# Optimization experiments

Hardware: AMD Instinct MI355X
Metric: run time of the kernel (lower is better)

Reference implementation:

```python
import jax, jax.numpy as jnp
import numpy as np


def setup_inputs() -> dict:
    key = jax.random.key(0)
    k1, k2, k3, k4 = jax.random.split(key, 4)
    B, C, T, H, W = 2, 64, 8, 48, 48
    C2 = C // 2
    x_in = jax.random.normal(k1, (B, C, T, H, W), dtype=jnp.float32)
    # per-time-slice 1x1 conv weights (theta/phi pairs), kaiming-ish scale
    theta_w = jax.random.normal(k2, (T, C2, C), dtype=jnp.float32) / np.sqrt(C)
    phi_w = jax.random.normal(k3, (T, C2, C), dtype=jnp.float32) / np.sqrt(C)
    out_w = jax.random.normal(k4, (C, C), dtype=jnp.float32) / np.sqrt(C)
    return {"x_in": x_in, "theta_w": theta_w, "phi_w": phi_w, "out_w": out_w}


def reference(x_in, theta_w, phi_w, out_w):
    B, C, T, H, W = x_in.shape
    C2 = theta_w.shape[1]
    P = H * W
    # [B, T, C, P] layout: flatten spatial, move time next to batch
    x = jnp.transpose(x_in, (0, 2, 1, 3, 4)).reshape(B, T, C, P)
    # per-slice 1x1 convs == per-slice channel matmuls with slice-specific weights
    theta = jnp.einsum("toc,btcp->btop", theta_w, x)  # [B,T,C2,P]
    phi = jnp.einsum("toc,btcp->btop", phi_w, x)      # [B,T,C2,P]
    scale = 1.0 / jnp.sqrt(jnp.asarray(C2, dtype=x_in.dtype))
    scores = jnp.einsum("btcp,btcq->btpq", theta, phi) * scale  # [B,T,P,P]
    attn = jax.nn.softmax(scores, axis=-1)
    f = jnp.einsum("btpq,btcq->btcp", attn, x)  # value = raw x, [B,T,C,P]
    # conv_out: 1x1x1 Conv3d (pointwise over channels), then residual
    out = jnp.einsum("oc,btcp->btop", out_w, f)
    out = jnp.transpose(out.reshape(B, T, C, H, W), (0, 2, 1, 3, 4))
    return out + x_in
```

## Files before the change

### kernel.cpp

```cpp
#include <hip/hip_runtime.h>
#include <hip/hip_bf16.h>

#define CC 64
#define TT 8
#define PP 2304
#define C2 32
#define BT 16
#define NKT 36
#define SCALE2 0.25503486f

using h8 = __attribute__((ext_vector_type(8))) _Float16;
using h4 = __attribute__((ext_vector_type(4))) _Float16;
using f4 = __attribute__((ext_vector_type(4))) float;

#if __has_builtin(__builtin_amdgcn_exp2f)
#define EXP2(v) __builtin_amdgcn_exp2f(v)
#else
#define EXP2(v) exp2f(v)
#endif

#define SWIZ_BT(xcd, g) ((xcd) + 8 * ((g) & 1))


__global__ __launch_bounds__(512) void k_prep(
    const float* __restrict__ x, const float* __restrict__ tw,
    const float* __restrict__ pw, _Float16* __restrict__ thf,
    _Float16* __restrict__ rec) {
  const int qt = blockIdx.y >> 1, bt = SWIZ_BT(blockIdx.x, blockIdx.y);
  const int b = bt >> 3, t = bt & 7;
  const int tid = threadIdx.x;
  const int wv = tid >> 6, lane = tid & 63;
  const int quad = lane >> 4, l15 = lane & 15;

  __shared__ __align__(16) float x_s[64][68];
  __shared__ __align__(16) _Float16 th_s[4][16][32];
  __shared__ __align__(16) _Float16 ph_s[4][16][32];

  const size_t xslice = ((size_t)b * CC * TT + t) * PP;
  const int qg0 = qt * 64;
  _Float16* rb = rec + (size_t)(bt * NKT + qt) * 6144;
  const f4 zero = {0.f, 0.f, 0.f, 0.f};

  {
    const int l16 = tid & 15;
    const int crow = tid >> 4;
#pragma unroll
    for (int ppass = 0; ppass < 2; ppass++) {
      const int c = ppass * 32 + crow;
      float4 u = *reinterpret_cast<const float4*>(
          &x[xslice + (size_t)c * (TT * PP) + qg0 + l16 * 4]);
      x_s[l16 * 4 + 0][c] = u.x;
      x_s[l16 * 4 + 1][c] = u.y;
      x_s[l16 * 4 + 2][c] = u.z;
      x_s[l16 * 4 + 3][c] = u.w;
    }
  }
  __syncthreads();

  if (wv < 4) {
    h8 bx[2];
#pragma unroll
    for (int ks = 0; ks < 2; ks++) {
      const float* row = &x_s[wv * 16 + l15][ks * 32 + quad * 8];
      float4 u0 = *reinterpret_cast<const float4*>(row);
      float4 u1 = *reinterpret_cast<const float4*>(row + 4);
      bx[ks][0] = (_Float16)u0.x; bx[ks][1] = (_Float16)u0.y;
      bx[ks][2] = (_Float16)u0.z; bx[ks][3] = (_Float16)u0.w;
      bx[ks][4] = (_Float16)u1.x; bx[ks][5] = (_Float16)u1.y;
      bx[ks][6] = (_Float16)u1.z; bx[ks][7] = (_Float16)u1.w;
    }

    const float* twt = tw + t * C2 * CC;
    const float* pwt = pw + t * C2 * CC;
    f4 accT[2] = {zero, zero}, accP[2] = {zero, zero};
#pragma unroll
    for (int mt = 0; mt < 2; mt++)
#pragma unroll
      for (int ks = 0; ks < 2; ks++) {
        const float* wr = twt + (mt * 16 + l15) * CC + ks * 32 + quad * 8;
        const float* pr = pwt + (mt * 16 + l15) * CC + ks * 32 + quad * 8;
        float4 a0 = *reinterpret_cast<const float4*>(wr);
        float4 a1 = *reinterpret_cast<const float4*>(wr + 4);
        float4 p0 = *reinterpret_cast<const float4*>(pr);
        float4 p1 = *reinterpret_cast<const float4*>(pr + 4);
        h8 at = {(_Float16)a0.x, (_Float16)a0.y, (_Float16)a0.z,
                 (_Float16)a0.w, (_Float16)a1.x, (_Float16)a1.y,
                 (_Float16)a1.z, (_Float16)a1.w};
        h8 ap = {(_Float16)p0.x, (_Float16)p0.y, (_Float16)p0.z,
                 (_Float16)p0.w, (_Float16)p1.x, (_Float16)p1.y,
                 (_Float16)p1.z, (_Float16)p1.w};
        accT[mt] = __builtin_amdgcn_mfma_f32_16x16x32_f16(at, bx[ks],
                                                          accT[mt], 0, 0, 0);
        accP[mt] = __builtin_amdgcn_mfma_f32_16x16x32_f16(ap, bx[ks],
                                                          accP[mt], 0, 0, 0);
      }

#pragma unroll
    for (int mt = 0; mt < 2; mt++) {
      h4 tv, pv;
#pragma unroll
      for (int r = 0; r < 4; r++) {
        tv[r] = (_Float16)(accT[mt][r] * SCALE2);
        pv[r] = (_Float16)accP[mt][r];
      }
      *reinterpret_cast<h4*>(&th_s[wv][l15][mt * 16 + quad * 4]) = tv;
      *reinterpret_cast<h4*>(&ph_s[wv][l15][mt * 16 + quad * 4]) = pv;
    }

    h8 tfrag = *reinterpret_cast<const h8*>(&th_s[wv][l15][quad * 8]);
    *reinterpret_cast<h8*>(
        thf + (((size_t)(bt * NKT + qt) * 4 + wv) * 64 + lane) * 8) = tfrag;

    h8 pfrag = *reinterpret_cast<const h8*>(&ph_s[wv][l15][quad * 8]);
    *reinterpret_cast<h8*>(rb + wv * 512 + lane * 8) = pfrag;
  } else {
    const int w2 = wv - 4;
    const int g = w2 >> 1;
#pragma unroll
    for (int ct2 = 0; ct2 < 2; ct2++) {
      const int ct = (w2 & 1) * 2 + ct2;
      h8 v;
#pragma unroll
      for (int j = 0; j < 4; j++) {
        v[j] = (_Float16)x_s[32 * g + quad * 4 + j][ct * 16 + l15];
        v[4 + j] = (_Float16)x_s[32 * g + 16 + quad * 4 + j][ct * 16 + l15];
      }
      *reinterpret_cast<h8*>(rb + 2048 + (g * 4 + ct) * 512 + lane * 8) = v;
    }
  }
}

__global__ __launch_bounds__(192, 3) void k_attn(
    const float* __restrict__ x, const _Float16* __restrict__ thf,
    const _Float16* __restrict__ rec, const float* __restrict__ ow,
    float* __restrict__ out) {
  const int strip = blockIdx.y >> 1;
  const int bt = SWIZ_BT(blockIdx.x, blockIdx.y);
  const int b = bt >> 3, t = bt & 7;
  const int tid = threadIdx.x;
  const int pf = tid >> 6, lane = tid & 63;
  const int quad = lane >> 4, l15 = lane & 15;

  const h8 bth = *reinterpret_cast<const h8*>(
      thf + (((size_t)bt * 144 + strip * 3 + pf) * 64 + lane) * 8);

  const _Float16* recb = rec + (size_t)bt * NKT * 6144 + lane * 8;

  const f4 zero = {0.f, 0.f, 0.f, 0.f};
  f4 O[4];
#pragma unroll
  for (int ct = 0; ct < 4; ct++) O[ct] = zero;
  float lsum = 0.f;

#pragma unroll 2
  for (int i = 0; i < NKT; i++) {
    const _Float16* _p = recb + (size_t)i * 6144;
    h8 buf[12];
#pragma unroll
    for (int j = 0; j < 12; j++)
      buf[j] = *reinterpret_cast<const h8*>(_p + j * 512);

    f4 s[4];
#pragma unroll
    for (int nt = 0; nt < 4; nt++)
      s[nt] =
          __builtin_amdgcn_mfma_f32_16x16x32_f16(buf[nt], bth, zero, 0, 0, 0);
#pragma unroll
    for (int g = 0; g < 2; g++) {
      h8 bw;
#pragma unroll
      for (int r = 0; r < 4; r++) {
        float w0 = EXP2(s[2 * g][r]);
        float w1 = EXP2(s[2 * g + 1][r]);
        lsum += w0 + w1;
        bw[r] = (_Float16)w0;
        bw[4 + r] = (_Float16)w1;
      }
#pragma unroll
      for (int ct = 0; ct < 4; ct++)
        O[ct] = __builtin_amdgcn_mfma_f32_16x16x32_f16(buf[4 + g * 4 + ct], bw,
                                                       O[ct], 0, 0, 0);
    }
  }

  lsum += __shfl_xor(lsum, 16);
  lsum += __shfl_xor(lsum, 32);
  const float inv = 1.f / lsum;

  h4 bf[4];
#pragma unroll
  for (int ct = 0; ct < 4; ct++)
#pragma unroll
    for (int r = 0; r < 4; r++) bf[ct][r] = (_Float16)(O[ct][r] * inv);

  f4 D3[4] = {zero, zero, zero, zero};
#pragma unroll
  for (int mt = 0; mt < 4; mt++)
#pragma unroll
    for (int ct = 0; ct < 4; ct++) {
      const float* wrow = ow + (size_t)(mt * 16 + l15) * CC + ct * 16 + quad * 4;
      float4 u = *reinterpret_cast<const float4*>(wrow);
      h4 aw = {(_Float16)u.x, (_Float16)u.y, (_Float16)u.z, (_Float16)u.w};
      D3[mt] = __builtin_amdgcn_mfma_f32_16x16x16f16(aw, bf[ct], D3[mt], 0, 0, 0);
    }

  const int p0 = strip * 48 + pf * 16 + l15;
#pragma unroll
  for (int mt = 0; mt < 4; mt++)
#pragma unroll
    for (int r = 0; r < 4; r++) {
      const int o = mt * 16 + quad * 4 + r;
      const size_t base = ((size_t)(b * CC + o) * TT + t) * PP + p0;
      out[base] = D3[mt][r] + x[base];
    }
}

extern "C" void kernel_launch(void* const* d_in, const int* in_sizes, int n_in,
                              void* d_out, int out_size, void* d_ws,
                              size_t ws_size, hipStream_t stream) {
  (void)in_sizes; (void)n_in; (void)out_size; (void)ws_size;
  const float* x = (const float*)d_in[0];
  const float* tw = (const float*)d_in[1];
  const float* pw = (const float*)d_in[2];
  const float* ow = (const float*)d_in[3];
  float* out = (float*)d_out;

  _Float16* thf = (_Float16*)d_ws;
  _Float16* rec = thf + (size_t)BT * NKT * 4 * 64 * 8;

  k_prep<<<dim3(8, 72), 512, 0, stream>>>(x, tw, pw, thf, rec);
  k_attn<<<dim3(8, 96), 192, 0, stream>>>(x, thf, rec, ow, out);
}
```

Before: 116.2 us.

## Split prep blocks in half and software-pipeline attention key tile loads

The prep kernel now handles 32 query positions per block with 256 threads, doubling the grid so more blocks can run at once. The attention loop replaces the single 12-fragment load per key tile with two half-tile buffers that are double-buffered. The next half is loaded while the current one runs through MFMA and exp. This is meant to hide global load latency and lower register pressure, at the cost of more loop bookkeeping and more blocks each reading the prep weights.

```diff
diff --git a/kernel.cpp b/kernel.cpp
--- a/kernel.cpp
+++ b/kernel.cpp
@@ -22,42 +22,44 @@
 #define SWIZ_BT(xcd, g) ((xcd) + 8 * ((g) & 1))
 
 
-__global__ __launch_bounds__(512) void k_prep(
+__global__ __launch_bounds__(256) void k_prep(
     const float* __restrict__ x, const float* __restrict__ tw,
     const float* __restrict__ pw, _Float16* __restrict__ thf,
     _Float16* __restrict__ rec) {
-  const int qt = blockIdx.y >> 1, bt = SWIZ_BT(blockIdx.x, blockIdx.y);
+  const int bt = SWIZ_BT(blockIdx.x, blockIdx.y);
+  const int qt = blockIdx.y >> 2;
+  const int g = (blockIdx.y >> 1) & 1;
   const int b = bt >> 3, t = bt & 7;
   const int tid = threadIdx.x;
   const int wv = tid >> 6, lane = tid & 63;
   const int quad = lane >> 4, l15 = lane & 15;
 
-  __shared__ __align__(16) float x_s[64][68];
-  __shared__ __align__(16) _Float16 th_s[4][16][32];
-  __shared__ __align__(16) _Float16 ph_s[4][16][32];
+  __shared__ __align__(16) float x_s[32][68];
+  __shared__ __align__(16) _Float16 th_s[2][16][32];
+  __shared__ __align__(16) _Float16 ph_s[2][16][32];
 
   const size_t xslice = ((size_t)b * CC * TT + t) * PP;
-  const int qg0 = qt * 64;
+  const int qg0 = qt * 64 + g * 32;
   _Float16* rb = rec + (size_t)(bt * NKT + qt) * 6144;
   const f4 zero = {0.f, 0.f, 0.f, 0.f};
 
   {
-    const int l16 = tid & 15;
-    const int crow = tid >> 4;
+    const int qoff = (tid & 7) * 4;
+    const int c0 = tid >> 3;
 #pragma unroll
     for (int ppass = 0; ppass < 2; ppass++) {
-      const int c = ppass * 32 + crow;
+      const int c = ppass * 32 + c0;
       float4 u = *reinterpret_cast<const float4*>(
-          &x[xslice + (size_t)c * (TT * PP) + qg0 + l16 * 4]);
-      x_s[l16 * 4 + 0][c] = u.x;
-      x_s[l16 * 4 + 1][c] = u.y;
-      x_s[l16 * 4 + 2][c] = u.z;
-      x_s[l16 * 4 + 3][c] = u.w;
+          &x[xslice + (size_t)c * (TT * PP) + qg0 + qoff]);
+      x_s[qoff + 0][c] = u.x;
+      x_s[qoff + 1][c] = u.y;
+      x_s[qoff + 2][c] = u.z;
+      x_s[qoff + 3][c] = u.w;
     }
   }
   __syncthreads();
 
-  if (wv < 4) {
+  if (wv < 2) {
     h8 bx[2];
 #pragma unroll
     for (int ks = 0; ks < 2; ks++) {
@@ -109,21 +111,21 @@
 
     h8 tfrag = *reinterpret_cast<const h8*>(&th_s[wv][l15][quad * 8]);
     *reinterpret_cast<h8*>(
-        thf + (((size_t)(bt * NKT + qt) * 4 + wv) * 64 + lane) * 8) = tfrag;
+        thf + (((size_t)(bt * 144 + qt * 4 + g * 2 + wv)) * 64 + lane) * 8) =
+        tfrag;
 
     h8 pfrag = *reinterpret_cast<const h8*>(&ph_s[wv][l15][quad * 8]);
-    *reinterpret_cast<h8*>(rb + wv * 512 + lane * 8) = pfrag;
+    *reinterpret_cast<h8*>(rb + (g * 2 + wv) * 512 + lane * 8) = pfrag;
   } else {
-    const int w2 = wv - 4;
-    const int g = w2 >> 1;
+    const int w2 = wv - 2;
 #pragma unroll
     for (int ct2 = 0; ct2 < 2; ct2++) {
-      const int ct = (w2 & 1) * 2 + ct2;
+      const int ct = w2 * 2 + ct2;
       h8 v;
 #pragma unroll
       for (int j = 0; j < 4; j++) {
-        v[j] = (_Float16)x_s[32 * g + quad * 4 + j][ct * 16 + l15];
-        v[4 + j] = (_Float16)x_s[32 * g + 16 + quad * 4 + j][ct * 16 + l15];
+        v[j] = (_Float16)x_s[quad * 4 + j][ct * 16 + l15];
+        v[4 + j] = (_Float16)x_s[16 + quad * 4 + j][ct * 16 + l15];
       }
       *reinterpret_cast<h8*>(rb + 2048 + (g * 4 + ct) * 512 + lane * 8) = v;
     }
@@ -152,36 +154,47 @@
   for (int ct = 0; ct < 4; ct++) O[ct] = zero;
   float lsum = 0.f;
 
+  h8 hA[6], hB[6];
+
+#define LOADH(BUF, i, gg)                                                    \
+  {                                                                          \
+    const _Float16* _p = recb + (size_t)(i)*6144;                            \
+    BUF[0] = *reinterpret_cast<const h8*>(_p + (2 * (gg)) * 512);            \
+    BUF[1] = *reinterpret_cast<const h8*>(_p + (2 * (gg) + 1) * 512);        \
+    _Pragma("unroll") for (int c = 0; c < 4; c++)                            \
+        BUF[2 + c] =                                                         \
+        *reinterpret_cast<const h8*>(_p + 2048 + ((gg)*4 + c) * 512);        \
+  }
+
+#define COMPH(BUF)                                                          \
+  {                                                                         \
+    f4 sA = __builtin_amdgcn_mfma_f32_16x16x32_f16(BUF[0], bth, zero, 0, 0, \
+                                                   0);                      \
+    f4 sB = __builtin_amdgcn_mfma_f32_16x16x32_f16(BUF[1], bth, zero, 0, 0, \
+                                                   0);                      \
+    h8 bw;                                                                  \
+    _Pragma("unroll") for (int r = 0; r < 4; r++) {                         \
+      float w0 = EXP2(sA[r]);                                               \
+      float w1 = EXP2(sB[r]);                                               \
+      lsum += w0 + w1;                                                      \
+      bw[r] = (_Float16)w0;                                                 \
+      bw[4 + r] = (_Float16)w1;                                             \
+    }                                                                       \
+    _Pragma("unroll") for (int ct = 0; ct < 4; ct++)                        \
+        O[ct] = __builtin_amdgcn_mfma_f32_16x16x32_f16(BUF[2 + ct], bw,     \
+                                                       O[ct], 0, 0, 0);     \
+  }
+
+  LOADH(hA, 0, 0);
 #pragma unroll 2
   for (int i = 0; i < NKT; i++) {
-    const _Float16* _p = recb + (size_t)i * 6144;
-    h8 buf[12];
-#pragma unroll
-    for (int j = 0; j < 12; j++)
-      buf[j] = *reinterpret_cast<const h8*>(_p + j * 512);
-
-    f4 s[4];
-#pragma unroll
-    for (int nt = 0; nt < 4; nt++)
-      s[nt] =
-          __builtin_amdgcn_mfma_f32_16x16x32_f16(buf[nt], bth, zero, 0, 0, 0);
-#pragma unroll
-    for (int g = 0; g < 2; g++) {
-      h8 bw;
-#pragma unroll
-      for (int r = 0; r < 4; r++) {
-        float w0 = EXP2(s[2 * g][r]);
-        float w1 = EXP2(s[2 * g + 1][r]);
-        lsum += w0 + w1;
-        bw[r] = (_Float16)w0;
-        bw[4 + r] = (_Float16)w1;
-      }
-#pragma unroll
-      for (int ct = 0; ct < 4; ct++)
-        O[ct] = __builtin_amdgcn_mfma_f32_16x16x32_f16(buf[4 + g * 4 + ct], bw,
-                                                       O[ct], 0, 0, 0);
-    }
-  }
+    LOADH(hB, i, 1);
+    COMPH(hA);
+    if (i + 1 < NKT) LOADH(hA, i + 1, 0);
+    COMPH(hB);
+  }
+#undef LOADH
+#undef COMPH
 
   lsum += __shfl_xor(lsum, 16);
   lsum += __shfl_xor(lsum, 32);
@@ -228,6 +241,6 @@
   _Float16* thf = (_Float16*)d_ws;
   _Float16* rec = thf + (size_t)BT * NKT * 4 * 64 * 8;
 
-  k_prep<<<dim3(8, 72), 512, 0, stream>>>(x, tw, pw, thf, rec);
+  k_prep<<<dim3(8, 144), 256, 0, stream>>>(x, tw, pw, thf, rec);
   k_attn<<<dim3(8, 96), 192, 0, stream>>>(x, thf, rec, ow, out);
 }
```

New measurement: 109.9 us. 1.06x faster.
